# Optimization experiments

Hardware: AMD Instinct MI355X
Metric: run time of the kernel (lower is better)

Reference implementation:

```python
import jax, jax.numpy as jnp
import numpy as np

NUM_HEADS = 32
NUM_KV_HEADS = 8
HEAD_DIM = 128
EPS = 1e-5
ROPE_THETA = 10000.0


def _rope(x, positions):
    # x: [S, H, D] (NeoX-style rotate-half), positions: [S] int
    half = HEAD_DIM // 2
    inv_freq = 1.0 / (ROPE_THETA ** (jnp.arange(0, HEAD_DIM, 2, dtype=jnp.float32) / HEAD_DIM))
    freqs = positions.astype(jnp.float32)[:, None] * inv_freq  # [S, half]
    cos = jnp.concatenate([jnp.cos(freqs), jnp.cos(freqs)], axis=-1)[:, None, :]  # [S,1,D]
    sin = jnp.concatenate([jnp.sin(freqs), jnp.sin(freqs)], axis=-1)[:, None, :]
    x1, x2 = x[..., :half], x[..., half:]
    rot = jnp.concatenate([-x2, x1], axis=-1)
    return x * cos + rot * sin


def setup_inputs() -> dict:
    key = jax.random.key(0)
    k1, k2, k3 = jax.random.split(key, 3)
    S, H = 2048, 4096
    q_size = NUM_HEADS * HEAD_DIM
    kv_size = NUM_KV_HEADS * HEAD_DIM
    return {
        "positions": jnp.arange(S, dtype=jnp.int32),
        "hidden_states": jax.random.normal(k1, (S, H), dtype=jnp.float32),
        "layernorm_weight": jnp.ones((H,), dtype=jnp.float32),
        "w_qkv": jax.random.normal(k2, (q_size + 2 * kv_size, H), dtype=jnp.float32) * (H ** -0.5),
        "w_o": jax.random.normal(k3, (H, q_size), dtype=jnp.float32) * (q_size ** -0.5),
    }


def reference(positions, hidden_states, layernorm_weight, w_qkv, w_o):
    S, H = hidden_states.shape
    # Fused RMSNorm (computed in f32) + QKV projection
    x32 = hidden_states.astype(jnp.float32)
    var = jnp.mean(x32 * x32, axis=-1, keepdims=True)
    xn = x32 * jax.lax.rsqrt(var + EPS) * layernorm_weight
    qkv = xn @ w_qkv.T  # [S, (Hq+2*Hkv)*D]
    q_size = NUM_HEADS * HEAD_DIM
    kv_size = NUM_KV_HEADS * HEAD_DIM
    q = qkv[:, :q_size].reshape(S, NUM_HEADS, HEAD_DIM)
    k = qkv[:, q_size:q_size + kv_size].reshape(S, NUM_KV_HEADS, HEAD_DIM)
    v = qkv[:, q_size + kv_size:].reshape(S, NUM_KV_HEADS, HEAD_DIM)
    # RoPE on q, k
    q = _rope(q, positions)
    k = _rope(k, positions)
    # GQA: expand kv heads to query heads
    group = NUM_HEADS // NUM_KV_HEADS
    k = jnp.repeat(k, group, axis=1)  # [S, Hq, D]
    v = jnp.repeat(v, group, axis=1)
    scale = HEAD_DIM ** -0.5
    scores = jnp.einsum('qhd,khd->hqk', q, k) * scale  # [Hq, S, S]
    mask = positions[:, None] >= positions[None, :]  # causal
    scores = jnp.where(mask[None, :, :], scores, jnp.finfo(scores.dtype).min)
    probs = jax.nn.softmax(scores, axis=-1)
    attn = jnp.einsum('hqk,khd->qhd', probs, v).reshape(S, q_size)
    out = attn @ w_o.T  # [S, H]
    return out.astype(hidden_states.dtype)
```

## Files before the change

### kernel.cpp

```cpp
#include <hip/hip_runtime.h>
#include <stdint.h>
#include <type_traits>


typedef __bf16 bf16x8 __attribute__((ext_vector_type(8)));
typedef float f32x4 __attribute__((ext_vector_type(4)));

#define S_LEN 2048
#define HDIM 4096
#define QKV_N 6144
#define NQH 32
#define NKVH 8
#define HD 128

__device__ __forceinline__ float bf2f(uint16_t u){
    union { uint32_t u; float f; } v; v.u = ((uint32_t)u) << 16; return v.f;
}
__device__ __forceinline__ uint16_t f2bf(float f){
    union { float f; uint32_t u; } v; v.f = f;
    uint32_t u = v.u;
    return (uint16_t)((u + 0x7FFFu + ((u >> 16) & 1u)) >> 16);
}

__device__ __forceinline__ void gload_lds16(uint16_t* lds_dst, const uint16_t* g_src){
    __builtin_amdgcn_global_load_lds(
        (const __attribute__((address_space(1))) void*)(g_src),
        (__attribute__((address_space(3))) void*)(lds_dst),
        16, 0, 0);
}

__device__ __forceinline__ void cast8(const float* __restrict__ src, uint16_t* __restrict__ dst, size_t i){
    float4 a = *(const float4*)(src + i);
    float4 c = *(const float4*)(src + i + 4);
    uint16_t o[8];
    o[0] = f2bf(a.x); o[1] = f2bf(a.y); o[2] = f2bf(a.z); o[3] = f2bf(a.w);
    o[4] = f2bf(c.x); o[5] = f2bf(c.y); o[6] = f2bf(c.z); o[7] = f2bf(c.w);
    *(uint4*)(dst + i) = *(uint4*)o;
}

__global__ __launch_bounds__(256) void prep_k(const float* __restrict__ w_qkv,
                                              const float* __restrict__ x,
                                              const float* __restrict__ lw,
                                              uint16_t* __restrict__ wqkv_b,
                                              uint16_t* __restrict__ xn){
    int b = blockIdx.x;
    int t = threadIdx.x;
    if (b < 12288){
        cast8(w_qkv, wqkv_b, (size_t)b * 2048 + t * 8);
        return;
    }
    int row = b - 12288;
    const float* xr = x + (size_t)row * HDIM + t * 16;
    float f[16];
#pragma unroll
    for (int p = 0; p < 4; ++p) *(float4*)(f + p * 4) = *(const float4*)(xr + p * 4);
    float ss = 0.f;
#pragma unroll
    for (int i = 0; i < 16; ++i) ss += f[i] * f[i];
#pragma unroll
    for (int off = 32; off > 0; off >>= 1) ss += __shfl_down(ss, off);
    __shared__ float red[4];
    if ((t & 63) == 0) red[t >> 6] = ss;
    __syncthreads();
    float tot = red[0] + red[1] + red[2] + red[3];
    float inv = rsqrtf(tot * (1.0f / HDIM) + 1e-5f);
    float wf[16];
#pragma unroll
    for (int p = 0; p < 4; ++p) *(float4*)(wf + p * 4) = *(const float4*)(lw + t * 16 + p * 4);
    uint16_t o[16];
#pragma unroll
    for (int i = 0; i < 16; ++i) o[i] = f2bf(f[i] * inv * wf[i]);
    uint16_t* outp = xn + (size_t)row * HDIM + t * 16;
    *(uint4*)(outp)     = *(uint4*)(o);
    *(uint4*)(outp + 8) = *(uint4*)(o + 8);
}

template <typename OutT>
__global__ __launch_bounds__(256, 2) void gemm_bt_k(const uint16_t* __restrict__ A,
                                                    const uint16_t* __restrict__ B,
                                                    OutT* __restrict__ C,
                                                    int M, int N, int K){
    __shared__ uint16_t lA[2][128 * 64];
    __shared__ uint16_t lB[2][128 * 64];
    int t = threadIdx.x;
    int lane = t & 63;
    int w = t >> 6;
    int wm = w >> 1, wn = w & 1;
    int quad = lane >> 4, ln = lane & 15;
    int tileM = blockIdx.y * 128, tileN = blockIdx.x * 128;

    f32x4 acc[4][4];
#pragma unroll
    for (int i = 0; i < 4; ++i)
#pragma unroll
      for (int j = 0; j < 4; ++j) acc[i][j] = (f32x4){0.f, 0.f, 0.f, 0.f};

    #define GSTAGE(K0, BUF)                                                         \
    {                                                                               \
        _Pragma("unroll")                                                           \
        for (int it = 0; it < 4; ++it){                                             \
            int pp = it * 256 + t;                                                  \
            int row = pp >> 3, cc = pp & 7;                                         \
            int gcc = cc ^ (row & 7);                                               \
            gload_lds16(&lA[BUF][pp * 8], A + (size_t)(tileM + row) * K + (K0) + gcc * 8); \
            gload_lds16(&lB[BUF][pp * 8], B + (size_t)(tileN + row) * K + (K0) + gcc * 8); \
        }                                                                           \
    }

    GSTAGE(0, 0);
    __syncthreads();

    for (int k0 = 0; k0 < K; k0 += 64){
        int cur = (k0 >> 6) & 1;
        if (k0 + 64 < K) GSTAGE(k0 + 64, cur ^ 1);

#pragma unroll
        for (int kk = 0; kk < 64; kk += 32){
            int cc = (kk + quad * 8) >> 3;
            bf16x8 aF[4], bF[4];
#pragma unroll
            for (int i = 0; i < 4; ++i){
                int ra = wm * 64 + i * 16 + ln;
                aF[i] = *(const bf16x8*)&lA[cur][ra * 64 + ((cc ^ (ra & 7)) * 8)];
                int rb = wn * 64 + i * 16 + ln;
                bF[i] = *(const bf16x8*)&lB[cur][rb * 64 + ((cc ^ (rb & 7)) * 8)];
            }
#pragma unroll
            for (int i = 0; i < 4; ++i)
#pragma unroll
                for (int j = 0; j < 4; ++j)
                    acc[i][j] = __builtin_amdgcn_mfma_f32_16x16x32_bf16(aF[i], bF[j], acc[i][j], 0, 0, 0);
        }
        __syncthreads();
    }
    #undef GSTAGE

#pragma unroll
    for (int i = 0; i < 4; ++i)
#pragma unroll
      for (int r = 0; r < 4; ++r){
          int row = tileM + wm * 64 + i * 16 + quad * 4 + r;
#pragma unroll
          for (int j = 0; j < 4; ++j){
              int col = tileN + wn * 64 + j * 16 + ln;
              if constexpr (std::is_same<OutT, float>::value)
                  C[(size_t)row * N + col] = acc[i][j][r];
              else
                  C[(size_t)row * N + col] = f2bf(acc[i][j][r]);
          }
      }
}

__global__ __launch_bounds__(256) void ropevt_k(const int* __restrict__ pos,
                                                uint16_t* __restrict__ qkv,
                                                uint16_t* __restrict__ vT){
    int b = blockIdx.x;
    int t = threadIdx.x;
    if (b < 2048){
        int s = b;
        float fpos = (float)pos[s];
        uint16_t* rowp = qkv + (size_t)s * QKV_N;
#pragma unroll
        for (int rep = 0; rep < 3; ++rep){
            int g = t + rep * 256;
            if (rep == 2 && t >= 128) break;
            int head = g >> 4;
            int i4 = (g & 15) * 4;
            int col = (head < NQH) ? head * HD : HDIM + (head - NQH) * HD;
            uint16_t* p1 = rowp + col + i4;
            uint16_t* p2 = p1 + 64;
            ushort4 u1 = *(ushort4*)p1;
            ushort4 u2 = *(ushort4*)p2;
            uint16_t e1[4] = {u1.x, u1.y, u1.z, u1.w};
            uint16_t e2[4] = {u2.x, u2.y, u2.z, u2.w};
            uint16_t o1[4], o2[4];
#pragma unroll
            for (int e = 0; e < 4; ++e){
                float j = (float)(i4 + e);
                float inv = __expf(j * -0.14391156831212787f);
                float fr = fpos * inv;
                float sn, c;
                __sincosf(fr, &sn, &c);
                float x1 = bf2f(e1[e]), x2 = bf2f(e2[e]);
                o1[e] = f2bf(x1 * c - x2 * sn);
                o2[e] = f2bf(x2 * c + x1 * sn);
            }
            *(ushort4*)p1 = make_ushort4(o1[0], o1[1], o1[2], o1[3]);
            *(ushort4*)p2 = make_ushort4(o2[0], o2[1], o2[2], o2[3]);
        }
        return;
    }
    __shared__ uint16_t tile[64][65];
    int bx = b - 2048;
    int ts = (bx & 31) * 64;
    int tc = (bx >> 5) * 64;
#pragma unroll
    for (int p = 0; p < 16; ++p){
        int lin = p * 256 + t;
        int r = lin >> 6, c = lin & 63;
        tile[r][c] = qkv[(size_t)(ts + r) * QKV_N + (HDIM + 1024) + tc + c];
    }
    __syncthreads();
#pragma unroll
    for (int p = 0; p < 16; ++p){
        int lin = p * 256 + t;
        int r = lin >> 6, c = lin & 63;
        vT[(size_t)(tc + r) * S_LEN + ts + c] = tile[c][r];
    }
}

__global__ __launch_bounds__(256, 2) void attn_k(const uint16_t* __restrict__ qkv,
                                                 const uint16_t* __restrict__ vT,
                                                 uint16_t* __restrict__ attn,
                                                 const float* __restrict__ w_o,
                                                 uint16_t* __restrict__ wo_b){
    int bid = blockIdx.x;
    int t = threadIdx.x;
    if (bid >= 512){
        cast8(w_o, wo_b, (size_t)(bid - 512) * 2048 + t * 8);
        return;
    }
    __shared__ uint16_t lK[2][64 * 128];
    __shared__ uint16_t lV[2][64 * 128];
    __shared__ uint16_t lP[4 * 2048];
    int h = bid & 31;
    int z = bid >> 5;
    int qt = (z < 8) ? 15 - z : z - 8;
    int kvh = h >> 2;
    int lane = t & 63, w = t >> 6;
    int quad = lane >> 4, ln = lane & 15;
    int qBase = qt * 128 + w * 32;

    const float scale = 0.088388347648318447f;

    bf16x8 qF[2][4];
#pragma unroll
    for (int i = 0; i < 2; ++i)
#pragma unroll
      for (int kk = 0; kk < 4; ++kk){
          int row = qBase + i * 16 + ln;
          bf16x8 raw = *(const bf16x8*)(qkv + (size_t)row * QKV_N + h * HD + kk * 32 + quad * 8);
#pragma unroll
          for (int e = 0; e < 8; ++e){
              union { __bf16 b; uint16_t u; } cv; cv.b = raw[e];
              union { uint16_t u; __bf16 b; } cw; cw.u = f2bf(bf2f(cv.u) * scale);
              raw[e] = cw.b;
          }
          qF[i][kk] = raw;
      }

    f32x4 oAcc[2][8];
#pragma unroll
    for (int i = 0; i < 2; ++i)
#pragma unroll
      for (int j = 0; j < 8; ++j) oAcc[i][j] = (f32x4){0.f, 0.f, 0.f, 0.f};
    float lsum[2][4];
#pragma unroll
    for (int i = 0; i < 2; ++i)
#pragma unroll
      for (int r = 0; r < 4; ++r) lsum[i][r] = 0.f;

    uint16_t* pB = lP + w * 2048;

    int nkt = 2 * qt + 2;

    #define STAGE(KT, B)                                                            \
    {                                                                               \
        _Pragma("unroll")                                                           \
        for (int it = 0; it < 4; ++it){                                             \
            int pp = it * 256 + t;                                                  \
            int row = pp >> 4, cc = pp & 15;                                        \
            int gcc = cc ^ (row & 7);                                               \
            gload_lds16(&lK[B][pp * 8],                                             \
                        qkv + (size_t)((KT) * 64 + row) * QKV_N + HDIM + kvh * HD + gcc * 8); \
            int rowv = pp >> 3, ccv = pp & 7;                                       \
            int gccv = ccv ^ (rowv & 7);                                            \
            gload_lds16(&lV[B][pp * 8],                                             \
                        vT + (size_t)(kvh * HD + rowv) * S_LEN + (KT) * 64 + gccv * 8); \
        }                                                                           \
    }

    STAGE(0, 0);
    __syncthreads();

    for (int kt = 0; kt < nkt; ++kt){
        int cur = kt & 1;
        if (kt + 1 < nkt) STAGE(kt + 1, cur ^ 1);

        f32x4 sAcc[2][4];
#pragma unroll
        for (int i = 0; i < 2; ++i)
#pragma unroll
          for (int j = 0; j < 4; ++j) sAcc[i][j] = (f32x4){0.f, 0.f, 0.f, 0.f};

#pragma unroll
        for (int kk = 0; kk < 4; ++kk){
            int cc = kk * 4 + quad;
            bf16x8 bF[4];
#pragma unroll
            for (int j = 0; j < 4; ++j){
                int row = j * 16 + ln;
                bF[j] = *(const bf16x8*)&lK[cur][row * 128 + ((cc ^ (row & 7)) * 8)];
            }
#pragma unroll
            for (int i = 0; i < 2; ++i)
#pragma unroll
              for (int j = 0; j < 4; ++j)
                  sAcc[i][j] = __builtin_amdgcn_mfma_f32_16x16x32_bf16(qF[i][kk], bF[j], sAcc[i][j], 0, 0, 0);
        }

        bool diag = (kt >= nkt - 2);
#pragma unroll
        for (int i = 0; i < 2; ++i)
#pragma unroll
          for (int r = 0; r < 4; ++r){
              int qrow = qBase + i * 16 + quad * 4 + r;
              int prow = i * 16 + quad * 4 + r;
              float part = 0.f;
#pragma unroll
              for (int j = 0; j < 4; ++j){
                  float sv = sAcc[i][j][r];
                  if (diag){
                      int colg = kt * 64 + j * 16 + ln;
                      if (colg > qrow) sv = -1e30f;
                  }
                  float pv = __expf(sv);
                  part += pv;
                  int colc = j * 16 + ln;
                  pB[prow * 64 + ((((colc >> 3) ^ (prow & 7)) & 7) * 8) + (colc & 7)] = f2bf(pv);
              }
              lsum[i][r] += part;
          }

#pragma unroll
        for (int kk = 0; kk < 2; ++kk){
            int cc = kk * 4 + quad;
            bf16x8 aP[2];
#pragma unroll
            for (int i = 0; i < 2; ++i){
                int row = i * 16 + ln;
                aP[i] = *(const bf16x8*)&pB[row * 64 + (((cc ^ (row & 7)) & 7) * 8)];
            }
            bf16x8 bV[8];
#pragma unroll
            for (int j = 0; j < 8; ++j){
                int row = j * 16 + ln;
                bV[j] = *(const bf16x8*)&lV[cur][row * 64 + (((cc ^ (row & 7)) & 7) * 8)];
            }
#pragma unroll
            for (int i = 0; i < 2; ++i)
#pragma unroll
              for (int j = 0; j < 8; ++j)
                  oAcc[i][j] = __builtin_amdgcn_mfma_f32_16x16x32_bf16(aP[i], bV[j], oAcc[i][j], 0, 0, 0);
        }

        __syncthreads();
    }
    #undef STAGE

#pragma unroll
    for (int i = 0; i < 2; ++i)
#pragma unroll
      for (int r = 0; r < 4; ++r){
          float l = lsum[i][r];
#pragma unroll
          for (int off = 1; off < 16; off <<= 1) l += __shfl_xor(l, off);
          float invl = 1.0f / l;
          int row = qBase + i * 16 + quad * 4 + r;
#pragma unroll
          for (int j = 0; j < 8; ++j)
              attn[(size_t)row * HDIM + h * HD + j * 16 + ln] = f2bf(oAcc[i][j][r] * invl);
      }
}

extern "C" void kernel_launch(void* const* d_in, const int* in_sizes, int n_in,
                              void* d_out, int out_size, void* d_ws, size_t ws_size,
                              hipStream_t stream){
    const int*   positions = (const int*)d_in[0];
    const float* hidden    = (const float*)d_in[1];
    const float* lw        = (const float*)d_in[2];
    const float* w_qkv     = (const float*)d_in[3];
    const float* w_o       = (const float*)d_in[4];
    float* out = (float*)d_out;

    uint16_t* xn     = (uint16_t*)d_ws;
    uint16_t* qkv    = xn     + (size_t)S_LEN * HDIM;
    uint16_t* vT     = qkv    + (size_t)S_LEN * QKV_N;
    uint16_t* attn   = vT     + (size_t)NKVH * HD * S_LEN;
    uint16_t* wqkv_b = attn   + (size_t)S_LEN * HDIM;
    uint16_t* wo_b   = wqkv_b + (size_t)QKV_N * HDIM;

    prep_k<<<14336, 256, 0, stream>>>(w_qkv, hidden, lw, wqkv_b, xn);
    gemm_bt_k<uint16_t><<<dim3(QKV_N / 128, S_LEN / 128), 256, 0, stream>>>(xn, wqkv_b, qkv, S_LEN, QKV_N, HDIM);
    ropevt_k<<<2560, 256, 0, stream>>>(positions, qkv, vT);
    attn_k<<<512 + 8192, 256, 0, stream>>>(qkv, vT, attn, w_o, wo_b);
    gemm_bt_k<float><<<dim3(HDIM / 128, S_LEN / 128), 256, 0, stream>>>(attn, wo_b, out, S_LEN, HDIM, HDIM);
}
```

Baseline: 475.5 us.

## Fuse fp32-to-bf16 weight conversion into GEMM B-tile loading

```diff
diff --git a/kernel.cpp b/kernel.cpp
--- a/kernel.cpp
+++ b/kernel.cpp
@@ -29,27 +29,11 @@
         16, 0, 0);
 }
 
-__device__ __forceinline__ void cast8(const float* __restrict__ src, uint16_t* __restrict__ dst, size_t i){
-    float4 a = *(const float4*)(src + i);
-    float4 c = *(const float4*)(src + i + 4);
-    uint16_t o[8];
-    o[0] = f2bf(a.x); o[1] = f2bf(a.y); o[2] = f2bf(a.z); o[3] = f2bf(a.w);
-    o[4] = f2bf(c.x); o[5] = f2bf(c.y); o[6] = f2bf(c.z); o[7] = f2bf(c.w);
-    *(uint4*)(dst + i) = *(uint4*)o;
-}
-
-__global__ __launch_bounds__(256) void prep_k(const float* __restrict__ w_qkv,
-                                              const float* __restrict__ x,
-                                              const float* __restrict__ lw,
-                                              uint16_t* __restrict__ wqkv_b,
-                                              uint16_t* __restrict__ xn){
-    int b = blockIdx.x;
+__global__ __launch_bounds__(256) void rmsnorm_k(const float* __restrict__ x,
+                                                 const float* __restrict__ lw,
+                                                 uint16_t* __restrict__ xn){
+    int row = blockIdx.x;
     int t = threadIdx.x;
-    if (b < 12288){
-        cast8(w_qkv, wqkv_b, (size_t)b * 2048 + t * 8);
-        return;
-    }
-    int row = b - 12288;
     const float* xr = x + (size_t)row * HDIM + t * 16;
     float f[16];
 #pragma unroll
@@ -77,7 +61,7 @@
 
 template <typename OutT>
 __global__ __launch_bounds__(256, 2) void gemm_bt_k(const uint16_t* __restrict__ A,
-                                                    const uint16_t* __restrict__ B,
+                                                    const float* __restrict__ Bf,
                                                     OutT* __restrict__ C,
                                                     int M, int N, int K){
     __shared__ uint16_t lA[2][128 * 64];
@@ -95,7 +79,9 @@
 #pragma unroll
       for (int j = 0; j < 4; ++j) acc[i][j] = (f32x4){0.f, 0.f, 0.f, 0.f};
 
-    #define GSTAGE(K0, BUF)                                                         \
+    float4 bPre[8];
+
+    #define ASTAGE(K0, BUF)                                                         \
     {                                                                               \
         _Pragma("unroll")                                                           \
         for (int it = 0; it < 4; ++it){                                             \
@@ -103,16 +89,45 @@
             int row = pp >> 3, cc = pp & 7;                                         \
             int gcc = cc ^ (row & 7);                                               \
             gload_lds16(&lA[BUF][pp * 8], A + (size_t)(tileM + row) * K + (K0) + gcc * 8); \
-            gload_lds16(&lB[BUF][pp * 8], B + (size_t)(tileN + row) * K + (K0) + gcc * 8); \
         }                                                                           \
     }
-
-    GSTAGE(0, 0);
+    #define BLOAD(K0)                                                               \
+    {                                                                               \
+        _Pragma("unroll")                                                           \
+        for (int it = 0; it < 4; ++it){                                             \
+            int pp = it * 256 + t;                                                  \
+            int row = pp >> 3, cc = pp & 7;                                         \
+            int gcc = cc ^ (row & 7);                                               \
+            const float* src = Bf + (size_t)(tileN + row) * K + (K0) + gcc * 8;     \
+            bPre[it * 2]     = *(const float4*)(src);                               \
+            bPre[it * 2 + 1] = *(const float4*)(src + 4);                           \
+        }                                                                           \
+    }
+    #define BSTORE(BUF)                                                             \
+    {                                                                               \
+        _Pragma("unroll")                                                           \
+        for (int it = 0; it < 4; ++it){                                             \
+            int pp = it * 256 + t;                                                  \
+            float4 a = bPre[it * 2], c = bPre[it * 2 + 1];                          \
+            uint16_t o[8];                                                          \
+            o[0] = f2bf(a.x); o[1] = f2bf(a.y); o[2] = f2bf(a.z); o[3] = f2bf(a.w); \
+            o[4] = f2bf(c.x); o[5] = f2bf(c.y); o[6] = f2bf(c.z); o[7] = f2bf(c.w); \
+            *(uint4*)&lB[BUF][pp * 8] = *(uint4*)o;                                 \
+        }                                                                           \
+    }
+
+    BLOAD(0);
+    ASTAGE(0, 0);
+    BSTORE(0);
     __syncthreads();
 
     for (int k0 = 0; k0 < K; k0 += 64){
         int cur = (k0 >> 6) & 1;
-        if (k0 + 64 < K) GSTAGE(k0 + 64, cur ^ 1);
+        bool more = (k0 + 64 < K);
+        if (more){
+            BLOAD(k0 + 64);
+            ASTAGE(k0 + 64, cur ^ 1);
+        }
 
 #pragma unroll
         for (int kk = 0; kk < 64; kk += 32){
@@ -131,9 +146,13 @@
                 for (int j = 0; j < 4; ++j)
                     acc[i][j] = __builtin_amdgcn_mfma_f32_16x16x32_bf16(aF[i], bF[j], acc[i][j], 0, 0, 0);
         }
+
+        if (more) BSTORE(cur ^ 1);
         __syncthreads();
     }
-    #undef GSTAGE
+    #undef ASTAGE
+    #undef BLOAD
+    #undef BSTORE
 
 #pragma unroll
     for (int i = 0; i < 4; ++i)
@@ -211,18 +230,12 @@
 
 __global__ __launch_bounds__(256, 2) void attn_k(const uint16_t* __restrict__ qkv,
                                                  const uint16_t* __restrict__ vT,
-                                                 uint16_t* __restrict__ attn,
-                                                 const float* __restrict__ w_o,
-                                                 uint16_t* __restrict__ wo_b){
-    int bid = blockIdx.x;
-    int t = threadIdx.x;
-    if (bid >= 512){
-        cast8(w_o, wo_b, (size_t)(bid - 512) * 2048 + t * 8);
-        return;
-    }
+                                                 uint16_t* __restrict__ attn){
     __shared__ uint16_t lK[2][64 * 128];
     __shared__ uint16_t lV[2][64 * 128];
     __shared__ uint16_t lP[4 * 2048];
+    int bid = blockIdx.x;
+    int t = threadIdx.x;
     int h = bid & 31;
     int z = bid >> 5;
     int qt = (z < 8) ? 15 - z : z - 8;
@@ -387,12 +400,10 @@
     uint16_t* qkv    = xn     + (size_t)S_LEN * HDIM;
     uint16_t* vT     = qkv    + (size_t)S_LEN * QKV_N;
     uint16_t* attn   = vT     + (size_t)NKVH * HD * S_LEN;
-    uint16_t* wqkv_b = attn   + (size_t)S_LEN * HDIM;
-    uint16_t* wo_b   = wqkv_b + (size_t)QKV_N * HDIM;
-
-    prep_k<<<14336, 256, 0, stream>>>(w_qkv, hidden, lw, wqkv_b, xn);
-    gemm_bt_k<uint16_t><<<dim3(QKV_N / 128, S_LEN / 128), 256, 0, stream>>>(xn, wqkv_b, qkv, S_LEN, QKV_N, HDIM);
+
+    rmsnorm_k<<<S_LEN, 256, 0, stream>>>(hidden, lw, xn);
+    gemm_bt_k<uint16_t><<<dim3(QKV_N / 128, S_LEN / 128), 256, 0, stream>>>(xn, w_qkv, qkv, S_LEN, QKV_N, HDIM);
     ropevt_k<<<2560, 256, 0, stream>>>(positions, qkv, vT);
-    attn_k<<<512 + 8192, 256, 0, stream>>>(qkv, vT, attn, w_o, wo_b);
-    gemm_bt_k<float><<<dim3(HDIM / 128, S_LEN / 128), 256, 0, stream>>>(attn, wo_b, out, S_LEN, HDIM, HDIM);
-}
+    attn_k<<<512, 256, 0, stream>>>(qkv, vT, attn);
+    gemm_bt_k<float><<<dim3(HDIM / 128, S_LEN / 128), 256, 0, stream>>>(attn, w_o, out, S_LEN, HDIM, HDIM);
+}
```

New measurement: 533.5 us. 1.12x slower.
